# Kernel tuning notes

Hardware: AMD Instinct MI355X
Metric: run time of the kernel (lower is better)

## Reference

```python
import jax, jax.numpy as jnp
import numpy as np

N_NODES = 100000
N_EDGES = 1600000
NFEAT = 128
NHID = 128


def setup_inputs() -> dict:
    key = jax.random.key(0)
    k1, k2, k3, k4 = jax.random.split(key, 4)
    x = jax.random.normal(k1, (N_NODES, NFEAT), dtype=jnp.float32)
    edge_index = jax.random.randint(k2, (2, N_EDGES), 0, N_NODES, dtype=jnp.int64)
    # GCNConv params (glorot-style scale)
    W1 = jax.random.normal(k3, (NFEAT, NHID), dtype=jnp.float32) * (1.0 / np.sqrt(NFEAT))
    b1 = jnp.zeros((NHID,), dtype=jnp.float32)
    return {"x": x, "edge_index": edge_index, "W1": W1, "b1": b1}


def gcn_conv(x, edge_index, W, b):
    # PyG GCNConv: out = D^{-1/2} (A + I) D^{-1/2} (x W) + b
    n = x.shape[0]
    loop = jnp.arange(n, dtype=edge_index.dtype)
    src = jnp.concatenate([edge_index[0], loop])  # message sources
    dst = jnp.concatenate([edge_index[1], loop])  # aggregation targets
    deg = jax.ops.segment_sum(jnp.ones_like(dst, dtype=x.dtype), dst, num_segments=n)
    dinv = jnp.where(deg > 0, jax.lax.rsqrt(deg), 0.0)
    norm = dinv[src] * dinv[dst]  # [E+N]
    h = x @ W  # [N, nhid]
    msg = h[src] * norm[:, None]  # gather + scale, [E+N, nhid]
    out = jax.ops.segment_sum(msg, dst, num_segments=n) + b
    return out


def reference(x, edge_index, W1, b1):
    # forward = gc1(x, edge_index) followed by dropout (identity in eval mode)
    return gcn_conv(x, edge_index, W1, b1)
```

## Files before the change

### kernel.cpp

```cpp
#include <hip/hip_runtime.h>
#include <math.h>


#define N_NODES 100000
#define N_EDGES 1600000
#define NF 128
#define LDW 136

#define BSHIFT 7
#define BNODES 128
#define NBUCK 782
#define ECAP 2432
#define CHUNK 4096
#define NCHUNK 391
#define GEMM_BLOCKS 1563

typedef short bf16x8 __attribute__((ext_vector_type(8)));
typedef float f32x4  __attribute__((ext_vector_type(4)));
typedef unsigned short u16;

__device__ inline u16 f2bf(float f) {
    unsigned int u = __float_as_uint(f);
    return (u16)((u + 0x7fffu + ((u >> 16) & 1u)) >> 16);
}

__device__ inline f32x4 unpk4u(unsigned int u) {
    f32x4 r;
    r[0] = (float)(u & 0xffu);
    r[1] = (float)((u >> 8) & 0xffu);
    r[2] = (float)((u >> 16) & 0xffu);
    r[3] = (float)((u >> 24) & 0xffu);
    return r;
}

__global__ __launch_bounds__(256) void prep_kernel(const float* __restrict__ W,
                                                   u16* __restrict__ Wimg,
                                                   int* __restrict__ bcur) {
    const int t = threadIdx.x;
    if (blockIdx.x == 0)
        for (int b = t; b < NBUCK; b += 256) bcur[b] = 0;
    for (int idx = blockIdx.x * 256 + t; idx < NF * NF; idx += 16 * 256) {
        int k = idx >> 7, n = idx & 127;
        Wimg[n * LDW + k] = f2bf(W[idx]);
    }
}

__global__ __launch_bounds__(256) void fused1_kernel(const float* __restrict__ x,
                                                     const u16* __restrict__ Wimg,
                                                     signed char* __restrict__ h8,
                                                     float* __restrict__ rscale,
                                                     const int* __restrict__ ei,
                                                     int* __restrict__ bcur,
                                                     unsigned int* __restrict__ ebuf) {
    __shared__ __align__(16) u16 Wt[NF * LDW];
    __shared__ __align__(16) u16 xs[64 * LDW];
    const int t = threadIdx.x;

    if (blockIdx.x >= GEMM_BLOCKS) {
        unsigned int* ed = (unsigned int*)Wt;
        int* cnt = (int*)((char*)Wt + 16384);
        int* cur = (int*)((char*)Wt + 16384 + 3200);
        unsigned int* es = (unsigned int*)xs;
        const int c = blockIdx.x - GEMM_BLOCKS;
        for (int b = t; b < NBUCK; b += 256) cnt[b] = 0;
        const int e0 = c * CHUNK;
        #pragma unroll 4
        for (int it = 0; it < CHUNK / 256; ++it) {
            int k = it * 256 + t;
            int e = e0 + k;
            if (e < N_EDGES) {
                ed[k] = (unsigned int)ei[N_EDGES + e];
                es[k] = (unsigned int)ei[e];
            } else ed[k] = 0xFFFFFFFFu;
        }
        __syncthreads();
        #pragma unroll 4
        for (int it = 0; it < CHUNK / 256; ++it) {
            unsigned int d = ed[it * 256 + t];
            if (d != 0xFFFFFFFFu) atomicAdd(&cnt[d >> BSHIFT], 1);
        }
        __syncthreads();
        for (int b = t; b < NBUCK; b += 256) {
            int v = cnt[b];
            cur[b] = b * ECAP + (v ? atomicAdd(&bcur[b], v) : 0);
        }
        __syncthreads();
        #pragma unroll 4
        for (int it = 0; it < CHUNK / 256; ++it) {
            int k = it * 256 + t;
            unsigned int d = ed[k];
            if (d != 0xFFFFFFFFu) {
                int pos = atomicAdd(&cur[d >> BSHIFT], 1);
                ebuf[pos] = ((d & (BNODES - 1u)) << 17) | es[k];
            }
        }
        return;
    }

    const int lane = t & 63;
    const int w = t >> 6;
    const int quad = lane >> 4;
    const int m = lane & 15;

    for (int idx = t; idx < (NF * LDW * 2) / 16; idx += 256)
        ((uint4*)Wt)[idx] = ((const uint4*)Wimg)[idx];

    const int rowbase = blockIdx.x * 64;
    for (int it = 0; it < 8; ++it) {
        int linear = it * 256 + t;
        int row = linear >> 5, colq = linear & 31;
        int grow = rowbase + row;
        float4 v = (grow < N_NODES) ? ((const float4*)x)[grow * 32 + colq]
                                    : make_float4(0.f, 0.f, 0.f, 0.f);
        unsigned a0 = (unsigned)f2bf(v.x) | ((unsigned)f2bf(v.y) << 16);
        unsigned a1 = (unsigned)f2bf(v.z) | ((unsigned)f2bf(v.w) << 16);
        *(uint2*)&xs[row * LDW + colq * 4] = make_uint2(a0, a1);
    }
    __syncthreads();

    f32x4 acc[8];
    #pragma unroll
    for (int nt = 0; nt < 8; ++nt) acc[nt] = (f32x4){0.f, 0.f, 0.f, 0.f};

    const int r0 = w * 16;
    #pragma unroll
    for (int kt = 0; kt < 4; ++kt) {
        const int k0 = kt * 32;
        bf16x8 a = *(const bf16x8*)&xs[(r0 + m) * LDW + k0 + quad * 8];
        #pragma unroll
        for (int nt = 0; nt < 8; ++nt) {
            bf16x8 bb = *(const bf16x8*)&Wt[(nt * 16 + m) * LDW + k0 + quad * 8];
            acc[nt] = __builtin_amdgcn_mfma_f32_16x16x32_bf16(a, bb, acc[nt], 0, 0, 0);
        }
    }

    float rmax[4];
    #pragma unroll
    for (int r = 0; r < 4; ++r) {
        float mx = 0.f;
        #pragma unroll
        for (int nt = 0; nt < 8; ++nt) mx = fmaxf(mx, fabsf(acc[nt][r]));
        #pragma unroll
        for (int off = 1; off < 16; off <<= 1) mx = fmaxf(mx, __shfl_xor(mx, off));
        rmax[r] = fmaxf(mx, 1e-20f);
    }

    __syncthreads();
    char* xs8 = (char*)xs;
    #pragma unroll
    for (int r = 0; r < 4; ++r) {
        const float inv = 127.f / rmax[r];
        const int row = r0 + quad * 4 + r;
        #pragma unroll
        for (int nt = 0; nt < 8; ++nt) {
            int q = __float2int_rn(acc[nt][r] * inv) + 128;
            xs8[row * 144 + nt * 16 + m] = (char)q;
        }
        if (m == 0) {
            int grow = rowbase + row;
            if (grow < N_NODES) rscale[grow] = rmax[r] * (1.f / 127.f);
        }
    }
    __syncthreads();

    for (int it = 0; it < 2; ++it) {
        int linear = it * 256 + t;
        int row = linear >> 3, seg = linear & 7;
        int grow = rowbase + row;
        if (grow < N_NODES) {
            uint4 v = *(const uint4*)&xs8[row * 144 + seg * 16];
            ((uint4*)h8)[grow * 8 + seg] = v;
        }
    }
}

__global__ __launch_bounds__(256) void fill3_kernel(unsigned int* __restrict__ ebuf,
                                                    const int* __restrict__ bcur,
                                                    const float* __restrict__ rscale,
                                                    float* __restrict__ combo,
                                                    int4* __restrict__ nodetab) {
    __shared__ unsigned int lde[ECAP];
    __shared__ int lcnt[BNODES];
    __shared__ int lsc[BNODES];
    __shared__ int lcur[BNODES];
    const int t = threadIdx.x, bkt = blockIdx.x;
    const int cnt = min(bcur[bkt], ECAP);
    const int gbase = bkt * ECAP;
    if (t < BNODES) lcnt[t] = 0;
    __syncthreads();
    for (int e = t; e < cnt; e += 256) {
        unsigned int p = ebuf[gbase + e];
        lde[e] = p;
        atomicAdd(&lcnt[p >> 17], 1);
    }
    __syncthreads();
    if (t < BNODES) lsc[t] = lcnt[t];
    __syncthreads();
    #pragma unroll
    for (int off = 1; off < BNODES; off <<= 1) {
        int v = (t < BNODES) ? lsc[t] : 0;
        int add = (t >= off && t < BNODES) ? lsc[t - off] : 0;
        __syncthreads();
        if (t < BNODES) lsc[t] = v + add;
        __syncthreads();
    }
    if (t < BNODES) {
        int c = lcnt[t];
        int startp = gbase + lsc[t] - c;
        lcur[t] = startp;
        int n = (bkt << BSHIFT) + t;
        if (n < N_NODES) {
            float dv = rsqrtf((float)c + 1.0f);
            float cb = dv * rscale[n];
            combo[n] = cb;
            nodetab[n] = make_int4(startp, c, __float_as_int(dv), __float_as_int(cb));
        }
    }
    __syncthreads();
    for (int e = t; e < cnt; e += 256) {
        unsigned int p = lde[e];
        int pos = atomicAdd(&lcur[p >> 17], 1);
        ebuf[pos] = p & 0x1ffffu;
    }
}

__global__ __launch_bounds__(256) void agg_kernel(const signed char* __restrict__ h8,
                                                  const float* __restrict__ combo,
                                                  const int4* __restrict__ nodetab,
                                                  const unsigned int* __restrict__ slot,
                                                  const float* __restrict__ b,
                                                  float* __restrict__ out) {
    const int wave = threadIdx.x >> 6;
    const int lane = threadIdx.x & 63;
    const int i = blockIdx.x * 4 + wave;
    if (i >= N_NODES) return;

    const int4 ni = nodetab[i];
    const int start = ni.x;
    const int m = ni.y;
    const float di = __int_as_float(ni.z);
    const float ci = __int_as_float(ni.w);
    const int half = lane >> 5;
    const int col = lane & 31;

    const unsigned int* h4 = (const unsigned int*)h8;
    f32x4 acc0 = {0.f, 0.f, 0.f, 0.f};
    f32x4 acc1 = {0.f, 0.f, 0.f, 0.f};
    float ws = 0.f;

    for (int base = 0; base < m; base += 64) {
        const int mm = min(m - base, 64);
        int   s_l  = (lane < mm) ? (int)slot[start + base + lane] : 0;
        float cw_l = (lane < mm) ? combo[s_l] : 0.0f;
        const int mu = (mm + 7) & ~7;
        for (int j = 0; j < mu; j += 8) {
            #pragma unroll
            for (int q = 0; q < 8; q += 2) {
                int   sj = __shfl(s_l,  j + q + half);
                float wj = __shfl(cw_l, j + q + half);
                unsigned int u = h4[sj * 32 + col];
                ws += wj;
                f32x4 hv = unpk4u(u);
                if (q & 2) acc1 += hv * wj;
                else       acc0 += hv * wj;
            }
        }
    }

    f32x4 acc = acc0 + acc1;
    #pragma unroll
    for (int c = 0; c < 4; ++c) acc[c] += __shfl_xor(acc[c], 32);
    ws += __shfl_xor(ws, 32);

    if (lane < 32) {
        unsigned int uv = h4[i * 32 + col];
        f32x4 hv = unpk4u(uv);
        float4 bb = ((const float4*)b)[col];
        const float corr = 128.f * (ws + ci);
        float4 o;
        o.x = bb.x + di * (acc[0] + ci * hv[0] - corr);
        o.y = bb.y + di * (acc[1] + ci * hv[1] - corr);
        o.z = bb.z + di * (acc[2] + ci * hv[2] - corr);
        o.w = bb.w + di * (acc[3] + ci * hv[3] - corr);
        ((float4*)out)[i * 32 + col] = o;
    }
}

extern "C" void kernel_launch(void* const* d_in, const int* in_sizes, int n_in,
                              void* d_out, int out_size, void* d_ws, size_t ws_size,
                              hipStream_t stream) {
    const float* x  = (const float*)d_in[0];
    const int*   ei = (const int*)d_in[1];
    const float* W  = (const float*)d_in[2];
    const float* b  = (const float*)d_in[3];
    float* out = (float*)d_out;

    signed char* h8 = (signed char*)d_ws;
    float* rscale = (float*)d_ws + 3300000;
    float* combo  = (float*)d_ws + 3500000;
    int4*  nodetab = (int4*)((int*)d_ws + 3700000);
    int*   bcur   = (int*)d_ws + 4150000;
    u16*   Wimg   = (u16*)((int*)d_ws + 4200000);
    unsigned int* ebuf = (unsigned int*)d_ws + 4300000;

    prep_kernel<<<16, 256, 0, stream>>>(W, Wimg, bcur);
    fused1_kernel<<<GEMM_BLOCKS + NCHUNK, 256, 0, stream>>>(x, Wimg, h8, rscale,
                                                            ei, bcur, ebuf);
    fill3_kernel<<<NBUCK, 256, 0, stream>>>(ebuf, bcur, rscale, combo, nodetab);
    agg_kernel<<<(N_NODES + 3) / 4, 256, 0, stream>>>(h8, combo, nodetab, ebuf, b, out);
}
```

Measured before the change: 198.9 us.

## Drop LDS staging of W and x in fused GEMM; read operands from global

The fused GEMM/bucketing kernel no longer stages the bf16 weight image and the converted x tile in LDS. Each wave loads its MFMA A-operand straight from x in global memory, converting to bf16 in registers, and reads B fragments straight from a now unpadded, row-major Wimg through the cache. The source-index staging buffer in the bucketing blocks is also removed and those indices are re-read from global. Shared memory per block shrinks to about 22 KB and launch bounds request 4 blocks per SM, aiming for higher occupancy and fewer barriers, at the cost of redundant global/L2 traffic for W and less coalesced x reads.

```diff
diff --git a/kernel.cpp b/kernel.cpp
--- a/kernel.cpp
+++ b/kernel.cpp
@@ -5,7 +5,6 @@
 #define N_NODES 100000
 #define N_EDGES 1600000
 #define NF 128
-#define LDW 136
 
 #define BSHIFT 7
 #define BNODES 128
@@ -40,38 +39,32 @@
     if (blockIdx.x == 0)
         for (int b = t; b < NBUCK; b += 256) bcur[b] = 0;
     for (int idx = blockIdx.x * 256 + t; idx < NF * NF; idx += 16 * 256) {
-        int k = idx >> 7, n = idx & 127;
-        Wimg[n * LDW + k] = f2bf(W[idx]);
-    }
-}
-
-__global__ __launch_bounds__(256) void fused1_kernel(const float* __restrict__ x,
-                                                     const u16* __restrict__ Wimg,
-                                                     signed char* __restrict__ h8,
-                                                     float* __restrict__ rscale,
-                                                     const int* __restrict__ ei,
-                                                     int* __restrict__ bcur,
-                                                     unsigned int* __restrict__ ebuf) {
-    __shared__ __align__(16) u16 Wt[NF * LDW];
-    __shared__ __align__(16) u16 xs[64 * LDW];
+        int n = idx >> 7, k = idx & 127;
+        Wimg[idx] = f2bf(W[k * NF + n]);
+    }
+}
+
+__global__ __launch_bounds__(256, 4) void fused1_kernel(const float* __restrict__ x,
+                                                        const u16* __restrict__ Wimg,
+                                                        signed char* __restrict__ h8,
+                                                        float* __restrict__ rscale,
+                                                        const int* __restrict__ ei,
+                                                        int* __restrict__ bcur,
+                                                        unsigned int* __restrict__ ebuf) {
+    __shared__ __align__(16) char smem[22656];
     const int t = threadIdx.x;
 
     if (blockIdx.x >= GEMM_BLOCKS) {
-        unsigned int* ed = (unsigned int*)Wt;
-        int* cnt = (int*)((char*)Wt + 16384);
-        int* cur = (int*)((char*)Wt + 16384 + 3200);
-        unsigned int* es = (unsigned int*)xs;
+        unsigned int* ed = (unsigned int*)smem;
+        int* cnt = (int*)(smem + 16384);
+        int* cur = (int*)(smem + 16384 + 3136);
         const int c = blockIdx.x - GEMM_BLOCKS;
         for (int b = t; b < NBUCK; b += 256) cnt[b] = 0;
         const int e0 = c * CHUNK;
         #pragma unroll 4
         for (int it = 0; it < CHUNK / 256; ++it) {
-            int k = it * 256 + t;
-            int e = e0 + k;
-            if (e < N_EDGES) {
-                ed[k] = (unsigned int)ei[N_EDGES + e];
-                es[k] = (unsigned int)ei[e];
-            } else ed[k] = 0xFFFFFFFFu;
+            int k = it * 256 + t, e = e0 + k;
+            ed[k] = (e < N_EDGES) ? (unsigned int)ei[N_EDGES + e] : 0xFFFFFFFFu;
         }
         __syncthreads();
         #pragma unroll 4
@@ -91,7 +84,7 @@
             unsigned int d = ed[k];
             if (d != 0xFFFFFFFFu) {
                 int pos = atomicAdd(&cur[d >> BSHIFT], 1);
-                ebuf[pos] = ((d & (BNODES - 1u)) << 17) | es[k];
+                ebuf[pos] = ((d & (BNODES - 1u)) << 17) | (unsigned int)ei[e0 + k];
             }
         }
         return;
@@ -101,35 +94,31 @@
     const int w = t >> 6;
     const int quad = lane >> 4;
     const int m = lane & 15;
-
-    for (int idx = t; idx < (NF * LDW * 2) / 16; idx += 256)
-        ((uint4*)Wt)[idx] = ((const uint4*)Wimg)[idx];
-
     const int rowbase = blockIdx.x * 64;
-    for (int it = 0; it < 8; ++it) {
-        int linear = it * 256 + t;
-        int row = linear >> 5, colq = linear & 31;
-        int grow = rowbase + row;
-        float4 v = (grow < N_NODES) ? ((const float4*)x)[grow * 32 + colq]
-                                    : make_float4(0.f, 0.f, 0.f, 0.f);
-        unsigned a0 = (unsigned)f2bf(v.x) | ((unsigned)f2bf(v.y) << 16);
-        unsigned a1 = (unsigned)f2bf(v.z) | ((unsigned)f2bf(v.w) << 16);
-        *(uint2*)&xs[row * LDW + colq * 4] = make_uint2(a0, a1);
-    }
-    __syncthreads();
+    const int r0 = w * 16;
+    const int arow = rowbase + r0 + m;
+    const bool rv = arow < N_NODES;
+    const float4* x4 = (const float4*)x;
 
     f32x4 acc[8];
     #pragma unroll
     for (int nt = 0; nt < 8; ++nt) acc[nt] = (f32x4){0.f, 0.f, 0.f, 0.f};
 
-    const int r0 = w * 16;
     #pragma unroll
     for (int kt = 0; kt < 4; ++kt) {
-        const int k0 = kt * 32;
-        bf16x8 a = *(const bf16x8*)&xs[(r0 + m) * LDW + k0 + quad * 8];
+        float4 xa = make_float4(0.f, 0.f, 0.f, 0.f), xb = xa;
+        if (rv) {
+            xa = x4[arow * 32 + kt * 8 + quad * 2];
+            xb = x4[arow * 32 + kt * 8 + quad * 2 + 1];
+        }
+        bf16x8 a;
+        a[0] = (short)f2bf(xa.x); a[1] = (short)f2bf(xa.y);
+        a[2] = (short)f2bf(xa.z); a[3] = (short)f2bf(xa.w);
+        a[4] = (short)f2bf(xb.x); a[5] = (short)f2bf(xb.y);
+        a[6] = (short)f2bf(xb.z); a[7] = (short)f2bf(xb.w);
         #pragma unroll
         for (int nt = 0; nt < 8; ++nt) {
-            bf16x8 bb = *(const bf16x8*)&Wt[(nt * 16 + m) * LDW + k0 + quad * 8];
+            bf16x8 bb = *(const bf16x8*)&Wimg[(nt * 16 + m) * NF + kt * 32 + quad * 8];
             acc[nt] = __builtin_amdgcn_mfma_f32_16x16x32_bf16(a, bb, acc[nt], 0, 0, 0);
         }
     }
@@ -145,8 +134,7 @@
         rmax[r] = fmaxf(mx, 1e-20f);
     }
 
-    __syncthreads();
-    char* xs8 = (char*)xs;
+    char* xs8 = smem;
     #pragma unroll
     for (int r = 0; r < 4; ++r) {
         const float inv = 127.f / rmax[r];
```

Measured after the change: 219.6 us. +10.4%, slower.
